# Kernel optimization log

Hardware: AMD Instinct MI355X
Metric: run time of the kernel (lower is better)

The kernel has to match this reference:

```python
import jax, jax.numpy as jnp
import numpy as np

TRIM_RATIO = 0.1
B, N, D_IN, D_H, N_OUT, D_OUT = 64, 1024, 512, 1024, 10, 1


def setup_inputs() -> dict:
    key = jax.random.key(0)
    ks = jax.random.split(key, 10)
    X = jax.random.normal(ks[0], (B, N, D_IN), dtype=jnp.float32)
    # ragged valid lengths in [N//2, N]; guarantees num_valid > 2*k for trim_ratio=0.1
    lengths = jax.random.randint(ks[1], (B,), N // 2, N + 1)
    mask = (jnp.arange(N)[None, :] < lengths[:, None]).astype(jnp.float32)
    s_in, s_h = 1.0 / np.sqrt(D_IN), 1.0 / np.sqrt(D_H)
    W1 = jax.random.uniform(ks[2], (D_IN, D_H), jnp.float32, -s_in, s_in)
    b1 = jax.random.uniform(ks[3], (D_H,), jnp.float32, -s_in, s_in)
    W2 = jax.random.uniform(ks[4], (D_H, D_H), jnp.float32, -s_h, s_h)
    b2 = jax.random.uniform(ks[5], (D_H,), jnp.float32, -s_h, s_h)
    W3 = jax.random.uniform(ks[6], (D_H, D_H), jnp.float32, -s_h, s_h)
    b3 = jax.random.uniform(ks[7], (D_H,), jnp.float32, -s_h, s_h)
    W4 = jax.random.uniform(ks[8], (D_H, N_OUT * D_OUT), jnp.float32, -s_h, s_h)
    b4 = jax.random.uniform(ks[9], (N_OUT * D_OUT,), jnp.float32, -s_h, s_h)
    return {"X": X, "mask": mask, "W1": W1, "b1": b1, "W2": W2, "b2": b2,
            "W3": W3, "b3": b3, "W4": W4, "b4": b4}


def reference(X, mask, W1, b1, W2, b2, W3, b3, W4, b4):
    # encode MLP: [B,N,D_IN] -> [B,N,D_H]
    encoded = jax.nn.relu(jnp.einsum('bni,ih->bnh', X, W1) + b1) @ W2 + b2
    masked = encoded * mask[..., None]
    num_valid = mask.sum(axis=-1).astype(jnp.int32)                 # [B]
    k = (num_valid.astype(jnp.float32) * TRIM_RATIO).astype(jnp.int32)  # floor, as int()
    # push invalid rows to +inf so valid elements occupy the first num_valid slots after sort
    padded = jnp.where(mask[..., None] > 0, masked, jnp.inf)
    sorted_v = jnp.sort(padded, axis=1)                             # per-column sort, [B,N,D_H]
    pos = jnp.arange(N)[None, :]
    keep = (pos >= k[:, None]) & (pos < (num_valid - k)[:, None])   # [B,N]
    summed = jnp.sum(jnp.where(keep[..., None], sorted_v, 0.0), axis=1)  # [B,D_H]
    denom = (num_valid - 2 * k).astype(jnp.float32)[:, None]
    aggregated = summed / denom                                     # trimmed mean
    # decode MLP
    out = jax.nn.relu(aggregated @ W3 + b3) @ W4 + b4               # [B, N_OUT*D_OUT]
    out = out.reshape(-1, N_OUT, D_OUT).squeeze(-1)                 # [B, N_OUT]
    return out
```

## Files before the change

kernel.cpp:

```cpp
#include <hip/hip_runtime.h>


typedef _Float16 half8  __attribute__((ext_vector_type(8)));
typedef _Float16 half4v __attribute__((ext_vector_type(4)));
typedef float    floatx4 __attribute__((ext_vector_type(4)));

#define GLD_LDS(g, l)                                                                     \
  __builtin_amdgcn_global_load_lds((const __attribute__((address_space(1))) void*)(g),    \
                                   (__attribute__((address_space(3))) void*)(l), 16, 0, 0)

__global__ void prep_nv(const float* __restrict__ mask, int* __restrict__ nv_arr,
                        int* __restrict__ k_arr) {
  int b = blockIdx.x, lane = threadIdx.x;
  const float4* mp = (const float4*)(mask + (b << 10));
  float s = 0.f;
#pragma unroll
  for (int i = 0; i < 4; ++i) {
    float4 v = mp[lane + i * 64];
    s += v.x + v.y + v.z + v.w;
  }
#pragma unroll
  for (int off = 32; off > 0; off >>= 1) s += __shfl_xor(s, off, 64);
  if (lane == 0) {
    int nv = (int)(s + 0.5f);
    int kk = (int)((float)nv * 0.1f);
    nv_arr[b] = nv;
    k_arr[b] = kk;
  }
}

__device__ __forceinline__ void transpose_body(const float* __restrict__ W,
                                               _Float16* __restrict__ WT, int R, int C,
                                               int r0, int c0, _Float16 (*tile)[65]) {
  for (int i = threadIdx.x; i < 4096; i += 256) {
    int r = i >> 6, c = i & 63;
    tile[r][c] = (_Float16)W[(size_t)(r0 + r) * C + c0 + c];
  }
  __syncthreads();
  for (int i = threadIdx.x; i < 4096; i += 256) {
    int c = i >> 6, r = i & 63;
    WT[(size_t)(c0 + c) * R + r0 + r] = tile[r][c];
  }
}

__global__ __launch_bounds__(256) void preprocess(
    const float* __restrict__ X, _Float16* __restrict__ X16,
    const float* __restrict__ W1, _Float16* __restrict__ W1T,
    const float* __restrict__ W2, _Float16* __restrict__ W2T,
    const int* __restrict__ nv_arr) {
  __shared__ _Float16 tile[64][65];
  int bid = blockIdx.x;
  if (bid < 16384) {
    int n0 = (bid << 2) & 1023;
    int batch = bid >> 8;
    int nv = nv_arr[batch];
    if (n0 >= ((nv + 127) & ~127)) return;
    int i = (bid * 256 + threadIdx.x) * 8;
    float4 a = *(const float4*)(X + i);
    float4 c = *(const float4*)(X + i + 4);
    half8 h;
    h[0] = (_Float16)a.x; h[1] = (_Float16)a.y; h[2] = (_Float16)a.z; h[3] = (_Float16)a.w;
    h[4] = (_Float16)c.x; h[5] = (_Float16)c.y; h[6] = (_Float16)c.z; h[7] = (_Float16)c.w;
    *(half8*)(X16 + i) = h;
  } else if (bid < 16384 + 128) {
    int id = bid - 16384;
    transpose_body(W1, W1T, 512, 1024, (id & 7) * 64, (id >> 3) * 64, tile);
  } else {
    int id = bid - 16512;
    transpose_body(W2, W2T, 1024, 1024, (id & 15) * 64, (id >> 4) * 64, tile);
  }
}

template <int KDIM, int MODE>
__global__ __launch_bounds__(256, 3) void gemm_kernel(
    const _Float16* __restrict__ Aop, const _Float16* __restrict__ Bop,
    const float* __restrict__ bias, const int* __restrict__ nv_arr,
    _Float16* __restrict__ outp) {
  __shared__ __align__(16) _Float16 ldsA[128 * 64];
  __shared__ __align__(16) _Float16 ldsB[128 * 64];
  int i0, j0;
  int bid = blockIdx.x;
  int fat = (((bid >> 6) << 3) | (bid & 7)) * 128;
  int thin = ((bid >> 3) & 7) * 128;
  if (MODE == 1) {
    i0 = thin; j0 = fat;
    if ((j0 & 1023) >= nv_arr[j0 >> 10]) return;
  } else {
    i0 = fat; j0 = thin;
    if ((i0 & 1023) >= nv_arr[i0 >> 10]) return;
  }
  const int t = threadIdx.x, lane = t & 63;
  const int wv = t >> 6, wi = wv & 1, wj = wv >> 1;
  const int lr = lane & 15, q = lane >> 4;

  floatx4 acc[4][4] = {};

  const int gch = (t & 7) ^ ((t >> 3) & 7);
  const _Float16* gA[4];
  const _Float16* gB[4];
  _Float16* lA[4];
  _Float16* lB[4];
#pragma unroll
  for (int r = 0; r < 4; ++r) {
    int row = r * 32 + (t >> 3);
    gA[r] = Aop + (size_t)(i0 + row) * KDIM + gch * 8;
    gB[r] = Bop + (size_t)(j0 + row) * KDIM + gch * 8;
    lA[r] = ldsA + (r * 256 + (t & ~63)) * 8;
    lB[r] = ldsB + (r * 256 + (t & ~63)) * 8;
  }

  int aoff[4], boff[4];
#pragma unroll
  for (int mi = 0; mi < 4; ++mi) {
    int row = wi * 64 + mi * 16 + lr;
    aoff[mi] = row * 64 + ((q ^ (row & 7)) * 8);
  }
#pragma unroll
  for (int nj = 0; nj < 4; ++nj) {
    int row = wj * 64 + nj * 16 + lr;
    boff[nj] = row * 64 + ((q ^ (row & 7)) * 8);
  }

  for (int kt = 0; kt < KDIM / 64; ++kt) {
#pragma unroll
    for (int r = 0; r < 4; ++r) GLD_LDS(gA[r], lA[r]);
#pragma unroll
    for (int r = 0; r < 4; ++r) GLD_LDS(gB[r], lB[r]);
#pragma unroll
    for (int r = 0; r < 4; ++r) { gA[r] += 64; gB[r] += 64; }
    __syncthreads();
#pragma unroll
    for (int kk = 0; kk < 2; ++kk) {
      half8 af[4], bf[4];
#pragma unroll
      for (int mi = 0; mi < 4; ++mi) af[mi] = *(const half8*)&ldsA[aoff[mi] ^ (kk * 32)];
#pragma unroll
      for (int nj = 0; nj < 4; ++nj) bf[nj] = *(const half8*)&ldsB[boff[nj] ^ (kk * 32)];
#pragma unroll
      for (int mi = 0; mi < 4; ++mi)
#pragma unroll
        for (int nj = 0; nj < 4; ++nj)
          acc[mi][nj] =
              __builtin_amdgcn_mfma_f32_16x16x32_f16(af[mi], bf[nj], acc[mi][nj], 0, 0, 0);
    }
    __syncthreads();
  }

  if (MODE == 1) {
#pragma unroll
    for (int mi = 0; mi < 4; ++mi) {
      int ih = i0 + wi * 64 + mi * 16 + q * 4;
      floatx4 bb = *(const floatx4*)&bias[ih];
#pragma unroll
      for (int nj = 0; nj < 4; ++nj) {
        int j = j0 + wj * 64 + nj * 16 + lr;
        floatx4 v = acc[mi][nj];
        half4v hv;
#pragma unroll
        for (int r = 0; r < 4; ++r) hv[r] = (_Float16)fmaxf(v[r] + bb[r], 0.f);
        *(half4v*)&outp[(size_t)j * 1024 + ih] = hv;
      }
    }
  } else {
#pragma unroll
    for (int nj = 0; nj < 4; ++nj) {
      int j = j0 + wj * 64 + nj * 16 + lr;
      float bj = bias[j];
#pragma unroll
      for (int mi = 0; mi < 4; ++mi) {
        int im = i0 + wi * 64 + mi * 16 + q * 4;
        int bb = im >> 10, n = im & 1023;
        floatx4 v = acc[mi][nj];
        half4v hv;
#pragma unroll
        for (int r = 0; r < 4; ++r) hv[r] = (_Float16)(v[r] + bj);
        *(half4v*)&outp[((size_t)bb << 20) + ((size_t)j << 10) + (size_t)n] = hv;
      }
    }
  }
}

#define NB 1024
__global__ __launch_bounds__(256) void trim_kernel(const _Float16* __restrict__ encT,
                                                   const int* __restrict__ nv_arr,
                                                   const int* __restrict__ k_arr,
                                                   float* __restrict__ agg) {
  __shared__ unsigned int cnt[4 * NB];
  int t = threadIdx.x, lane = t & 63, w = t >> 6;
  int blk = blockIdx.x;
  int batch = blk >> 8;
  int h = ((blk & 255) << 2) + w;
  unsigned int* cw = cnt + w * NB;
  uint4* cp = (uint4*)cw;
  {
    uint4 z = {0u, 0u, 0u, 0u};
#pragma unroll
    for (int i = 0; i < 4; ++i) cp[lane * 4 + (i ^ ((lane >> 1) & 3))] = z;
  }

  int nv = nv_arr[batch], kk = k_arr[batch];
  const _Float16* col = encT + ((size_t)batch << 20) + ((size_t)h << 10);
  const uint4* p = (const uint4*)col + lane * 2;
  uint4 u0 = p[0], u1 = p[1];
  unsigned vals[8] = {u0.x, u0.y, u0.z, u0.w, u1.x, u1.y, u1.z, u1.w};
  int nvalid = nv - lane * 16;

  float vv[16];
  int bn[16];
#pragma unroll
  for (int d = 0; d < 8; ++d) {
    unsigned u = vals[d];
#pragma unroll
    for (int sub = 0; sub < 2; ++sub) {
      int idx = d * 2 + sub;
      unsigned short bits = (unsigned short)(sub ? (u >> 16) : (u & 0xffffu));
      _Float16 hvv;
      __builtin_memcpy(&hvv, &bits, 2);
      float v = (float)hvv;
      if (idx < nvalid) {
        v = fminf(fmaxf(v, -8.0f), 7.999f);
        int bin = (int)((v + 8.0f) * 64.0f);
        bin = min(NB - 1, bin);
        vv[idx] = v;
        bn[idx] = bin;
        int Lb = bin >> 4, jc = (bin >> 2) & 3;
        int phys = ((Lb << 2) + (jc ^ ((Lb >> 1) & 3))) * 4 + (bin & 3);
        atomicAdd(&cw[phys], 1u);
      } else {
        vv[idx] = 0.f;
        bn[idx] = -1;
      }
    }
  }

  int c[16];
  {
    uint4 rb[4];
#pragma unroll
    for (int i = 0; i < 4; ++i) rb[i] = cp[lane * 4 + (i ^ ((lane >> 1) & 3))];
#pragma unroll
    for (int i = 0; i < 4; ++i) {
      c[4 * i] = (int)rb[i].x; c[4 * i + 1] = (int)rb[i].y;
      c[4 * i + 2] = (int)rb[i].z; c[4 * i + 3] = (int)rb[i].w;
    }
  }
  int ct = 0;
#pragma unroll
  for (int i = 0; i < 16; ++i) ct += c[i];
  int ci = ct;
#pragma unroll
  for (int off = 1; off < 64; off <<= 1) {
    int cu = __shfl_up(ci, off, 64);
    if (lane >= off) ci += cu;
  }
  int cex = ci - ct;
  int r1 = kk, r2 = nv - kk;
  int p1 = -1, p2 = -1;
  {
    int run = cex;
#pragma unroll
    for (int i = 0; i < 16; ++i) {
      int cc = c[i];
      if (run < r1 && r1 <= run + cc) p1 = ((lane * 16 + i) << 12) | run;
      if (run < r2 && r2 <= run + cc) p2 = ((lane * 16 + i) << 12) | run;
      run += cc;
    }
  }
#pragma unroll
  for (int off = 32; off > 0; off >>= 1) {
    p1 = max(p1, __shfl_xor(p1, off, 64));
    p2 = max(p2, __shfl_xor(p2, off, 64));
  }
  int b1 = p1 >> 12, cex1 = p1 & 4095;
  int b2 = p2 >> 12, cex2 = p2 & 4095;
  float s1 = 0.f, s2 = 0.f, tm = 0.f;
  int c1 = 0, c2 = 0;
#pragma unroll
  for (int i = 0; i < 16; ++i) {
    int b = bn[i];
    float v = vv[i];
    if (b == b1) { s1 += v; c1++; }
    if (b == b2) { s2 += v; c2++; }
    if (b > b1 && b < b2) tm += v;
  }
#pragma unroll
  for (int off = 32; off > 0; off >>= 1) {
    s1 += __shfl_xor(s1, off, 64);
    s2 += __shfl_xor(s2, off, 64);
    tm += __shfl_xor(tm, off, 64);
    c1 += __shfl_xor(c1, off, 64);
    c2 += __shfl_xor(c2, off, 64);
  }
  float mid;
  if (b1 == b2) {
    mid = (float)(r2 - r1) * (s1 / (float)c1);
  } else {
    mid = (float)(cex1 + c1 - r1) * (s1 / (float)c1) + tm +
          (float)(r2 - cex2) * (s2 / (float)c2);
  }
  if (lane == 0) {
    agg[(batch << 10) + h] = mid / (float)(nv - 2 * kk);
  }
}

__global__ __launch_bounds__(256) void decode1(const float* __restrict__ agg,
                                               const float* __restrict__ W3,
                                               const float* __restrict__ b3,
                                               float* __restrict__ A3) {
  __shared__ float al[1024];
  __shared__ float red[256];
  int b = blockIdx.x, hb = blockIdx.y, t = threadIdx.x;
  for (int i = t; i < 1024; i += 256) al[i] = agg[(b << 10) + i];
  __syncthreads();
  int hl = t & 63, ks = t >> 6;
  int h = hb * 64 + hl;
  const float* wp = W3 + (size_t)(ks * 256) * 1024 + h;
  const float* ap = al + ks * 256;
  float acc = 0.f;
#pragma unroll 8
  for (int k = 0; k < 256; ++k) acc = fmaf(ap[k], wp[(size_t)k * 1024], acc);
  red[t] = acc;
  __syncthreads();
  if (t < 64) {
    float s = red[t] + red[t + 64] + red[t + 128] + red[t + 192] + b3[hb * 64 + t];
    A3[(b << 10) + hb * 64 + t] = fmaxf(s, 0.f);
  }
}

__global__ void decode2(const float* __restrict__ A3, const float* __restrict__ W4,
                        const float* __restrict__ b4, float* __restrict__ outp) {
  __shared__ float red[4][10];
  int b = blockIdx.x, t = threadIdx.x, lane = t & 63, w = t >> 6;
  float part[10];
#pragma unroll
  for (int o = 0; o < 10; ++o) part[o] = 0.f;
#pragma unroll
  for (int jj = 0; jj < 4; ++jj) {
    int h2 = jj * 256 + t;
    float a = A3[(b << 10) + h2];
#pragma unroll
    for (int o = 0; o < 10; ++o) part[o] = fmaf(a, W4[h2 * 10 + o], part[o]);
  }
#pragma unroll
  for (int o = 0; o < 10; ++o)
#pragma unroll
    for (int off = 32; off > 0; off >>= 1) part[o] += __shfl_xor(part[o], off, 64);
  if (lane == 0)
#pragma unroll
    for (int o = 0; o < 10; ++o) red[w][o] = part[o];
  __syncthreads();
  if (t < 10) outp[b * 10 + t] = b4[t] + red[0][t] + red[1][t] + red[2][t] + red[3][t];
}

extern "C" void kernel_launch(void* const* d_in, const int* in_sizes, int n_in,
                              void* d_out, int out_size, void* d_ws, size_t ws_size,
                              hipStream_t stream) {
  const float* X = (const float*)d_in[0];
  const float* mask = (const float*)d_in[1];
  const float* W1 = (const float*)d_in[2];
  const float* b1 = (const float*)d_in[3];
  const float* W2 = (const float*)d_in[4];
  const float* b2 = (const float*)d_in[5];
  const float* W3 = (const float*)d_in[6];
  const float* b3 = (const float*)d_in[7];
  const float* W4 = (const float*)d_in[8];
  const float* b4 = (const float*)d_in[9];
  float* outp = (float*)d_out;
  char* ws = (char*)d_ws;

  _Float16* X16 = (_Float16*)(ws);
  _Float16* H1 = (_Float16*)(ws + 67108864ull);
  _Float16* encT = (_Float16*)(ws + 201326592ull);
  _Float16* W1T = (_Float16*)(ws + 335544320ull);
  _Float16* W2T = (_Float16*)(ws + 336592896ull);
  float* agg = (float*)(ws + 338690048ull);
  float* A3 = (float*)(ws + 338952192ull);
  int* nv_arr = (int*)(ws + 339214336ull);
  int* k_arr = (int*)(ws + 339214592ull);

  prep_nv<<<64, 64, 0, stream>>>(mask, nv_arr, k_arr);
  preprocess<<<16768, 256, 0, stream>>>(X, X16, W1, W1T, W2, W2T, nv_arr);
  gemm_kernel<512, 1><<<4096, 256, 0, stream>>>(W1T, X16, b1, nv_arr, H1);
  gemm_kernel<1024, 2><<<4096, 256, 0, stream>>>(H1, W2T, b2, nv_arr, encT);
  trim_kernel<<<16384, 256, 0, stream>>>(encT, nv_arr, k_arr, agg);
  decode1<<<dim3(64, 16), 256, 0, stream>>>(agg, W3, b3, A3);
  decode2<<<64, 256, 0, stream>>>(A3, W4, b4, outp);
}
```

Measured before the change: 517.1 us.

## Rewrite GEMMs as 256x256 tiles with 512 threads and double-buffered LDS pipeline

Both encoder GEMMs now use 256x256 output tiles computed by 512-thread blocks (8 waves, each 128x64), instead of 128x128 tiles with 256 threads. Global-to-LDS loads for the next k-step are interleaved with MFMA phases through a double-buffered LDS scheme, with explicit barriers, waitcnt and setprio, so memory latency overlaps compute. The preprocess valid-row rounding widens to 256 to match the larger tile granularity. This raises operand reuse and cuts per-tile overhead, at the cost of heavy register and LDS use (128 KB), lower occupancy, and more wasted compute on ragged tails.

```diff
diff --git a/kernel.cpp b/kernel.cpp
--- a/kernel.cpp
+++ b/kernel.cpp
@@ -54,7 +54,7 @@
     int n0 = (bid << 2) & 1023;
     int batch = bid >> 8;
     int nv = nv_arr[batch];
-    if (n0 >= ((nv + 127) & ~127)) return;
+    if (n0 >= ((nv + 255) & ~255)) return;
     int i = (bid * 256 + threadIdx.x) * 8;
     float4 a = *(const float4*)(X + i);
     float4 c = *(const float4*)(X + i + 4);
@@ -72,16 +72,17 @@
 }
 
 template <int KDIM, int MODE>
-__global__ __launch_bounds__(256, 3) void gemm_kernel(
+__global__ __launch_bounds__(512, 2) void gemm_kernel(
     const _Float16* __restrict__ Aop, const _Float16* __restrict__ Bop,
     const float* __restrict__ bias, const int* __restrict__ nv_arr,
     _Float16* __restrict__ outp) {
-  __shared__ __align__(16) _Float16 ldsA[128 * 64];
-  __shared__ __align__(16) _Float16 ldsB[128 * 64];
+  constexpr int NT = KDIM / 64;
+  __shared__ __align__(16) _Float16 lds[2][2][256 * 64];
+
+  int bid = blockIdx.x;
+  int fat = ((((bid >> 5) << 3) | (bid & 7))) << 8;
+  int thin = ((bid >> 3) & 3) << 8;
   int i0, j0;
-  int bid = blockIdx.x;
-  int fat = (((bid >> 6) << 3) | (bid & 7)) * 128;
-  int thin = ((bid >> 3) & 7) * 128;
   if (MODE == 1) {
     i0 = thin; j0 = fat;
     if ((j0 & 1023) >= nv_arr[j0 >> 10]) return;
@@ -90,70 +91,92 @@
     if ((i0 & 1023) >= nv_arr[i0 >> 10]) return;
   }
   const int t = threadIdx.x, lane = t & 63;
-  const int wv = t >> 6, wi = wv & 1, wj = wv >> 1;
+  const int wv = t >> 6, wm = wv & 1, wn = wv >> 1;
   const int lr = lane & 15, q = lane >> 4;
-
-  floatx4 acc[4][4] = {};
+  const int swz = (q ^ (lr & 7)) * 8;
 
   const int gch = (t & 7) ^ ((t >> 3) & 7);
-  const _Float16* gA[4];
-  const _Float16* gB[4];
-  _Float16* lA[4];
-  _Float16* lB[4];
-#pragma unroll
-  for (int r = 0; r < 4; ++r) {
-    int row = r * 32 + (t >> 3);
-    gA[r] = Aop + (size_t)(i0 + row) * KDIM + gch * 8;
-    gB[r] = Bop + (size_t)(j0 + row) * KDIM + gch * 8;
-    lA[r] = ldsA + (r * 256 + (t & ~63)) * 8;
-    lB[r] = ldsB + (r * 256 + (t & ~63)) * 8;
-  }
-
-  int aoff[4], boff[4];
-#pragma unroll
-  for (int mi = 0; mi < 4; ++mi) {
-    int row = wi * 64 + mi * 16 + lr;
-    aoff[mi] = row * 64 + ((q ^ (row & 7)) * 8);
-  }
-#pragma unroll
-  for (int nj = 0; nj < 4; ++nj) {
-    int row = wj * 64 + nj * 16 + lr;
-    boff[nj] = row * 64 + ((q ^ (row & 7)) * 8);
-  }
-
-  for (int kt = 0; kt < KDIM / 64; ++kt) {
-#pragma unroll
-    for (int r = 0; r < 4; ++r) GLD_LDS(gA[r], lA[r]);
-#pragma unroll
-    for (int r = 0; r < 4; ++r) GLD_LDS(gB[r], lB[r]);
-#pragma unroll
-    for (int r = 0; r < 4; ++r) { gA[r] += 64; gB[r] += 64; }
-    __syncthreads();
-#pragma unroll
-    for (int kk = 0; kk < 2; ++kk) {
-      half8 af[4], bf[4];
-#pragma unroll
-      for (int mi = 0; mi < 4; ++mi) af[mi] = *(const half8*)&ldsA[aoff[mi] ^ (kk * 32)];
-#pragma unroll
-      for (int nj = 0; nj < 4; ++nj) bf[nj] = *(const half8*)&ldsB[boff[nj] ^ (kk * 32)];
-#pragma unroll
-      for (int mi = 0; mi < 4; ++mi)
-#pragma unroll
-        for (int nj = 0; nj < 4; ++nj)
-          acc[mi][nj] =
-              __builtin_amdgcn_mfma_f32_16x16x32_f16(af[mi], bf[nj], acc[mi][nj], 0, 0, 0);
-    }
-    __syncthreads();
-  }
+  const _Float16* gA = Aop + (size_t)(i0 + (t >> 3)) * KDIM + gch * 8;
+  const _Float16* gB = Bop + (size_t)(j0 + (t >> 3)) * KDIM + gch * 8;
+
+#define STG(OP, BUF, KT, R)                                                   \
+  GLD_LDS(((OP) ? gB : gA) + (size_t)(R) * 64 * KDIM + (size_t)(KT) * 64,     \
+          &lds[BUF][OP][((R) * 512 + (t & ~63)) * 8])
+
+  floatx4 acc[8][4] = {};
+  half8 af[4][2];
+  half8 bf[2][2][2];
+
+#define LD_A(BUF, IH)                                                         \
+  _Pragma("unroll") for (int f = 0; f < 4; ++f)                               \
+  _Pragma("unroll") for (int kk = 0; kk < 2; ++kk)                            \
+      af[f][kk] = *(const half8*)&lds[BUF][0]                                 \
+          [(((wm << 7) + ((IH) << 6) + (f << 4) + lr) << 6) + (swz ^ (kk << 5))];
+
+#define LD_B(BUF, JH)                                                         \
+  _Pragma("unroll") for (int g = 0; g < 2; ++g)                               \
+  _Pragma("unroll") for (int kk = 0; kk < 2; ++kk)                            \
+      bf[JH][g][kk] = *(const half8*)&lds[BUF][1]                             \
+          [(((wn << 6) + ((JH) << 5) + (g << 4) + lr) << 6) + (swz ^ (kk << 5))];
+
+#define MFMA_QUAD(IH, JH)                                                     \
+  _Pragma("unroll") for (int f = 0; f < 4; ++f)                               \
+  _Pragma("unroll") for (int g = 0; g < 2; ++g)                               \
+  _Pragma("unroll") for (int kk = 0; kk < 2; ++kk)                            \
+      acc[((IH) << 2) + f][((JH) << 1) + g] =                                 \
+          __builtin_amdgcn_mfma_f32_16x16x32_f16(                             \
+              af[f][kk], bf[JH][g][kk], acc[((IH) << 2) + f][((JH) << 1) + g], 0, 0, 0);
+
+#define PHASE_TAIL(IH, JH)                                                    \
+  __builtin_amdgcn_s_barrier();                                               \
+  asm volatile("s_waitcnt lgkmcnt(0)" ::: "memory");                          \
+  __builtin_amdgcn_sched_barrier(0);                                          \
+  __builtin_amdgcn_s_setprio(1);                                              \
+  MFMA_QUAD(IH, JH);                                                          \
+  __builtin_amdgcn_s_setprio(0);                                              \
+  __builtin_amdgcn_s_barrier();
+
+#define BODY(KT, CUR, NXT, DO_A, DO_B, VMC)                                   \
+  {                                                                           \
+    LD_A(CUR, 0); LD_B(CUR, 0);                                               \
+    if (DO_A) { STG(0, NXT, (KT) + 1, 0); STG(0, NXT, (KT) + 1, 1); }         \
+    PHASE_TAIL(0, 0);                                                         \
+    LD_B(CUR, 1);                                                             \
+    if (DO_A) { STG(0, NXT, (KT) + 1, 2); STG(0, NXT, (KT) + 1, 3); }         \
+    PHASE_TAIL(0, 1);                                                         \
+    LD_A(CUR, 1);                                                             \
+    if (DO_B) { STG(1, CUR, (KT) + 2, 0); STG(1, CUR, (KT) + 2, 1); }         \
+    PHASE_TAIL(1, 0);                                                         \
+    if (DO_B) { STG(1, CUR, (KT) + 2, 2); STG(1, CUR, (KT) + 2, 3); }         \
+    asm volatile("s_waitcnt " VMC ::: "memory");                              \
+    __builtin_amdgcn_sched_barrier(0);                                        \
+    __builtin_amdgcn_s_setprio(1);                                            \
+    MFMA_QUAD(1, 1);                                                          \
+    __builtin_amdgcn_s_setprio(0);                                            \
+    __builtin_amdgcn_s_barrier();                                             \
+  }
+
+  STG(0, 0, 0, 0); STG(0, 0, 0, 1); STG(0, 0, 0, 2); STG(0, 0, 0, 3);
+  STG(1, 0, 0, 0); STG(1, 0, 0, 1); STG(1, 0, 0, 2); STG(1, 0, 0, 3);
+  STG(1, 1, 1, 0); STG(1, 1, 1, 1); STG(1, 1, 1, 2); STG(1, 1, 1, 3);
+  asm volatile("s_waitcnt vmcnt(4)" ::: "memory");
+  __builtin_amdgcn_s_barrier();
+
+  for (int kt = 0; kt < NT - 3; kt += 2) {
+    BODY(kt, 0, 1, 1, 1, "vmcnt(4)");
+    BODY(kt + 1, 1, 0, 1, 1, "vmcnt(4)");
+  }
+  BODY(NT - 2, 0, 1, 1, 0, "vmcnt(0)");
+  BODY(NT - 1, 1, 0, 0, 0, "vmcnt(0)");
 
   if (MODE == 1) {
 #pragma unroll
-    for (int mi = 0; mi < 4; ++mi) {
-      int ih = i0 + wi * 64 + mi * 16 + q * 4;
+    for (int mi = 0; mi < 8; ++mi) {
+      int ih = i0 + (wm << 7) + (mi << 4) + (q << 2);
       floatx4 bb = *(const floatx4*)&bias[ih];
 #pragma unroll
       for (int nj = 0; nj < 4; ++nj) {
-        int j = j0 + wj * 64 + nj * 16 + lr;
+        int j = j0 + (wn << 6) + (nj << 4) + lr;
         floatx4 v = acc[mi][nj];
         half4v hv;
 #pragma unroll
@@ -164,11 +187,11 @@
   } else {
 #pragma unroll
     for (int nj = 0; nj < 4; ++nj) {
-      int j = j0 + wj * 64 + nj * 16 + lr;
+      int j = j0 + (wn << 6) + (nj << 4) + lr;
       float bj = bias[j];
 #pragma unroll
-      for (int mi = 0; mi < 4; ++mi) {
-        int im = i0 + wi * 64 + mi * 16 + q * 4;
+      for (int mi = 0; mi < 8; ++mi) {
+        int im = i0 + (wm << 7) + (mi << 4) + (q << 2);
         int bb = im >> 10, n = im & 1023;
         floatx4 v = acc[mi][nj];
         half4v hv;
@@ -380,8 +403,8 @@
 
   prep_nv<<<64, 64, 0, stream>>>(mask, nv_arr, k_arr);
   preprocess<<<16768, 256, 0, stream>>>(X, X16, W1, W1T, W2, W2T, nv_arr);
-  gemm_kernel<512, 1><<<4096, 256, 0, stream>>>(W1T, X16, b1, nv_arr, H1);
-  gemm_kernel<1024, 2><<<4096, 256, 0, stream>>>(H1, W2T, b2, nv_arr, encT);
+  gemm_kernel<512, 1><<<1024, 512, 0, stream>>>(W1T, X16, b1, nv_arr, H1);
+  gemm_kernel<1024, 2><<<1024, 512, 0, stream>>>(H1, W2T, b2, nv_arr, encT);
   trim_kernel<<<16384, 256, 0, stream>>>(encT, nv_arr, k_arr, agg);
   decode1<<<dim3(64, 16), 256, 0, stream>>>(agg, W3, b3, A3);
   decode2<<<64, 256, 0, stream>>>(A3, W4, b4, outp);
```

Result: slower. 535.2 us (+3.5%).
